# Performance work log

Hardware: AMD Instinct MI355X
Metric: run time of the kernel (lower is better)

The kernel has to match this reference:

```python
import jax, jax.numpy as jnp
import numpy as np
import math

MAX_LEN = 65536
NUM_HEADS = 16
HEAD_DIM = 64
K_MAX = 64
LOCAL_WINDOW = 512
LOG_N = math.ceil(math.log2(MAX_LEN + 1))   # 17
LEAF_START = 2 ** LOG_N                      # segment-tree leaf offset


def cover_set(pos):
    """O(log n) segment-tree nodes covering prefix [0..pos-1], each with leaf-depth."""
    if pos <= 0:
        return []
    l, r = LEAF_START, LEAF_START + min(pos, MAX_LEN)
    out = []
    while l < r:
        if l & 1:
            out.append((l, LOG_N - int(math.floor(math.log2(l)))))
            l += 1
        if r & 1:
            r -= 1
            out.append((r, LOG_N - int(math.floor(math.log2(r)))))
        l >>= 1
        r >>= 1
    return out


def node_content(v_tokens, node_idx, depth):
    """Content of a FULL subtree node under the concat/pairwise-mean gated merge.
    Equals: concat tokens while K<=k_max, then (left+right)/2 elementwise, which
    collapses to a strided mean over chunks of size L//K_MAX. Returns (H, K, D)."""
    L = 1 << depth
    a = (node_idx << depth) - LEAF_START          # first token covered by node
    chunk = v_tokens[a:a + L]                     # (L, H, D), static slice
    if L <= K_MAX:
        f = chunk                                 # (L, H, D)
    else:
        f = chunk.reshape(L // K_MAX, K_MAX, NUM_HEADS, HEAD_DIM).mean(0)  # (K_MAX,H,D)
    return jnp.transpose(f, (1, 0, 2))            # (H, K, D)


def setup_inputs() -> dict:
    key = jax.random.key(0)
    k1, k2, k3 = jax.random.split(key, 3)
    v_tokens = jax.random.normal(k1, (50000, NUM_HEADS, HEAD_DIM), jnp.float32)
    q_new = jax.random.normal(k2, (1, NUM_HEADS, HEAD_DIM), jnp.float32)
    depth_proj_w = jax.random.normal(k3, (LOG_N + 1, HEAD_DIM, HEAD_DIM), jnp.float32) * 0.02
    depth_temp = jnp.linspace(0.5, 4.0, LOG_N + 1).astype(jnp.float32)
    return {"v_tokens": v_tokens, "q_new": q_new, "depth_proj_w": depth_proj_w,
            "depth_temp": depth_temp, "n_tokens": 50000}


def reference(v_tokens, q_new, depth_proj_w, depth_temp, n_tokens):
    pos = int(n_tokens)
    q = q_new[0]                                   # (H, D)
    inv_sqrt_d = 1.0 / math.sqrt(HEAD_DIM)

    # --- local window attention over last min(pos, W) tokens (chronological) ---
    n_local = min(pos, LOCAL_WINDOW)
    v_local = v_tokens[pos - n_local:pos]          # (W, H, D)
    s = jnp.einsum('hd,khd->hk', q, v_local) * inv_sqrt_d
    w = jax.nn.softmax(s, axis=-1)
    local_out = jnp.einsum('hk,khd->hd', w, v_local)   # (H, D)

    # --- multi-depth causal tree attention over the O(log n) cover set ---
    node_outs = []
    for node_idx, depth in cover_set(pos):
        f = node_content(v_tokens, node_idx, depth)    # (H, K, D)
        q_depth = q + q @ depth_proj_w[depth].T        # depth-specific query delta
        scale = 1.0 / ((jax.nn.softplus(depth_temp[depth]) + 1e-6) * math.sqrt(HEAD_DIM))
        s = jnp.einsum('hd,hkd->hk', q_depth, f) * scale
        w = jnp.einsum('hk,hkd->hd', jax.nn.softmax(s, axis=-1), f)
        node_outs.append(w)
    if node_outs:
        tree_out = jnp.stack(node_outs, axis=0).mean(0)
    else:
        tree_out = jnp.zeros_like(local_out)

    return (local_out + tree_out)[None]            # (1, H, D)
```

## Files before the change

### kernel.cpp

```cpp
#include <hip/hip_runtime.h>
#include <math.h>

#define NUM_HEADS   16
#define HEAD_DIM    64
#define KMAXN       64
#define LOCAL_WIN   512
#define LOG_N       17
#define LEAF_START  131072
#define MAX_LEN_TOK 65536
#define ROW         1024
#define SLICE       65536
#define MAXN        34

typedef float vf4 __attribute__((ext_vector_type(4)));

__device__ __forceinline__ vf4 ntload(const float* p) {
    return __builtin_nontemporal_load((const vf4*)p);
}

struct K1Args {
    int nNodes;
    int a[MAXN];
    int cpb[MAXN];
    int C[MAXN];
    int CB[MAXN];
    int K[MAXN];
    int off[MAXN];
    int bbase[MAXN];
};

struct K2Args {
    int nNodes;
    int K[MAXN];
    int C[MAXN];
    int CB[MAXN];
    int off[MAXN];
    int depth[MAXN];
};

__device__ __forceinline__ void f4add(float4& a, const float4& b) {
    a.x += b.x; a.y += b.y; a.z += b.z; a.w += b.w;
}

__global__ __launch_bounds__(256, 4) void k1_reduce(const float* __restrict__ v,
                                                    float* __restrict__ ws,
                                                    K1Args A) {
    int b = blockIdx.x;
    int node = 0;
    for (int i = 1; i < A.nNodes; ++i)
        if (b >= A.bbase[i]) node = i;
    int lb  = b - A.bbase[node];
    int K   = A.K[node];
    int kgc = (K + 3) >> 2;
    int cb  = lb / kgc;
    int kg  = lb - cb * kgc;
    int k0  = kg * 4;
    int RK  = K - k0; if (RK > 4) RK = 4;
    int c0  = cb * A.cpb[node];
    int c1  = c0 + A.cpb[node];
    int C   = A.C[node];
    if (c1 > C) c1 = C;

    int j4 = threadIdx.x * 4;

    vf4 acc0 = 0.f, acc1 = 0.f, acc2 = 0.f, acc3 = 0.f;

    if (RK == 4) {
        int c = c0;
        for (; c + 2 <= c1; c += 2) {
            const float* p0 = v + (long)(A.a[node] + c * 64 + k0) * ROW + j4;
            const float* p1 = p0 + SLICE;
            vf4 y0 = ntload(p0);
            vf4 y1 = ntload(p0 + ROW);
            vf4 y2 = ntload(p0 + 2 * ROW);
            vf4 y3 = ntload(p0 + 3 * ROW);
            vf4 z0 = ntload(p1);
            vf4 z1 = ntload(p1 + ROW);
            vf4 z2 = ntload(p1 + 2 * ROW);
            vf4 z3 = ntload(p1 + 3 * ROW);
            acc0 += y0 + z0; acc1 += y1 + z1; acc2 += y2 + z2; acc3 += y3 + z3;
        }
        if (c < c1) {
            const float* p0 = v + (long)(A.a[node] + c * 64 + k0) * ROW + j4;
            acc0 += ntload(p0);
            acc1 += ntload(p0 + ROW);
            acc2 += ntload(p0 + 2 * ROW);
            acc3 += ntload(p0 + 3 * ROW);
        }
    } else {
        for (int c = c0; c < c1; ++c) {
            const float* p0 = v + (long)(A.a[node] + c * 64 + k0) * ROW + j4;
            if (RK > 0) acc0 += ntload(p0);
            if (RK > 1) acc1 += ntload(p0 + ROW);
            if (RK > 2) acc2 += ntload(p0 + 2 * ROW);
            if (RK > 3) acc3 += ntload(p0 + 3 * ROW);
        }
    }

    float* wp = ws + (long)A.off[node] + (long)cb * SLICE + (long)k0 * ROW + j4;
    if (RK > 0) *(vf4*)(wp)           = acc0;
    if (RK > 1) *(vf4*)(wp + ROW)     = acc1;
    if (RK > 2) *(vf4*)(wp + 2 * ROW) = acc2;
    if (RK > 3) *(vf4*)(wp + 3 * ROW) = acc3;
}

__global__ __launch_bounds__(256) void k1b_finalize(const float* __restrict__ ws_in,
                                                    float* __restrict__ f,
                                                    K2Args A) {
    int node = blockIdx.y;
    int k    = blockIdx.x;
    if (k >= A.K[node]) return;
    int CB = A.CB[node];
    const float* pf = ws_in + (long)A.off[node] + (long)k * ROW + threadIdx.x * 4;
    float4 a0 = make_float4(0.f,0.f,0.f,0.f);
    float4 a1 = a0, a2 = a0, a3 = a0;
    int cb = 0;
    for (; cb + 4 <= CB; cb += 4) {
        f4add(a0, *(const float4*)(pf + (long)cb * SLICE));
        f4add(a1, *(const float4*)(pf + (long)(cb+1) * SLICE));
        f4add(a2, *(const float4*)(pf + (long)(cb+2) * SLICE));
        f4add(a3, *(const float4*)(pf + (long)(cb+3) * SLICE));
    }
    for (; cb < CB; ++cb) f4add(a0, *(const float4*)(pf + (long)cb * SLICE));
    f4add(a0,a1); f4add(a2,a3); f4add(a0,a2);
    float invC = 1.0f / (float)A.C[node];
    a0.x*=invC; a0.y*=invC; a0.z*=invC; a0.w*=invC;
    *(float4*)(f + ((long)node * 64 + k) * ROW + threadIdx.x * 4) = a0;
}

__global__ __launch_bounds__(256) void k2_node_attn(const float* __restrict__ f,
                                                    const float* __restrict__ q,
                                                    const float* __restrict__ W,
                                                    const float* __restrict__ temp,
                                                    float* __restrict__ node_out,
                                                    K2Args A) {
    int h    = blockIdx.x;
    int node = blockIdx.y;
    int lane = threadIdx.x & 63;
    int w    = threadIdx.x >> 6;
    int K    = A.K[node];
    int dep  = A.depth[node];
    const float* pf = f + (long)node * SLICE + h * 64;

    __shared__ float qs[64], qds[64], sv[64], ps[64];
    __shared__ float red[4][64];

    if (threadIdx.x < 64) qs[lane] = q[h * 64 + lane];
    __syncthreads();

    float qp = 0.f;
    const float* Wr = W + ((long)dep * 64 + lane) * 64;
    #pragma unroll
    for (int e = w * 16; e < w * 16 + 16; ++e) qp += qs[e] * Wr[e];
    red[w][lane] = qp;
    __syncthreads();
    if (w == 0) qds[lane] = qs[lane] + red[0][lane] + red[1][lane] + red[2][lane] + red[3][lane];
    __syncthreads();
    float qd = qds[lane];

    float sp    = log1pf(expf(temp[dep]));
    float scale = 1.0f / ((sp + 1e-6f) * 8.0f);

    for (int k = w; k < K; k += 4) {
        float p = qd * pf[(long)k * ROW + lane];
        #pragma unroll
        for (int m = 1; m < 64; m <<= 1) p += __shfl_xor(p, m, 64);
        if (lane == 0) sv[k] = p * scale;
    }
    __syncthreads();

    if (w == 0) {
        float s  = (lane < K) ? sv[lane] : -1e30f;
        float mx = s;
        #pragma unroll
        for (int m = 1; m < 64; m <<= 1) mx = fmaxf(mx, __shfl_xor(mx, m, 64));
        float e = (lane < K) ? expf(s - mx) : 0.f;
        float S = e;
        #pragma unroll
        for (int m = 1; m < 64; m <<= 1) S += __shfl_xor(S, m, 64);
        ps[lane] = e / S;
    }
    __syncthreads();

    float o = 0.f;
    for (int k = w; k < K; k += 4) o += ps[k] * pf[(long)k * ROW + lane];
    red[w][lane] = o;
    __syncthreads();
    if (w == 0)
        node_out[node * ROW + h * 64 + lane] =
            red[0][lane] + red[1][lane] + red[2][lane] + red[3][lane];
}

__global__ __launch_bounds__(512) void k3_local(const float* __restrict__ v,
                                                const float* __restrict__ q,
                                                const float* __restrict__ node_out,
                                                int nNodes, int pos,
                                                float* __restrict__ out) {
    int h    = blockIdx.x;
    int tid  = threadIdx.x;
    int lane = tid & 63;
    int w    = tid >> 6;
    int nloc = pos < LOCAL_WIN ? pos : LOCAL_WIN;
    int t0   = pos - nloc;

    __shared__ float qs[64];
    __shared__ float sc[LOCAL_WIN];
    __shared__ float red[8][64];
    __shared__ float wred[16];
    __shared__ float mS[2];

    if (tid < 64) qs[tid] = q[h * 64 + tid];
    __syncthreads();

    float s = -1e30f;
    if (tid < nloc) {
        const float* vr = v + (long)(t0 + tid) * ROW + h * 64;
        float acc = 0.f;
        #pragma unroll 8
        for (int d = 0; d < 64; ++d) acc += qs[d] * vr[d];
        s = acc * 0.125f;
    }
    float mx = s;
    #pragma unroll
    for (int m = 1; m < 64; m <<= 1) mx = fmaxf(mx, __shfl_xor(mx, m, 64));
    if (lane == 0) wred[w] = mx;
    __syncthreads();
    if (tid == 0) {
        float m2 = wred[0];
        for (int i = 1; i < 8; ++i) m2 = fmaxf(m2, wred[i]);
        mS[0] = m2;
    }
    __syncthreads();
    float m = mS[0];

    float e = (tid < nloc) ? expf(s - m) : 0.f;
    sc[tid] = e;
    float su = e;
    #pragma unroll
    for (int mm = 1; mm < 64; mm <<= 1) su += __shfl_xor(su, mm, 64);
    if (lane == 0) wred[8 + w] = su;
    __syncthreads();
    if (tid == 0) {
        float S2 = 0.f;
        for (int i = 0; i < 8; ++i) S2 += wred[8 + i];
        mS[1] = S2;
    }
    __syncthreads();
    float S = mS[1];

    float acc = 0.f;
    {
        const float* vb = v + (long)t0 * ROW + h * 64 + lane;
        int tb = w * 64;
        #pragma unroll 4
        for (int i = 0; i < 64; ++i) {
            int t = tb + i;
            if (t < nloc) acc += sc[t] * vb[(long)t * ROW];
        }
    }
    red[w][lane] = acc;
    __syncthreads();

    if (w == 0) {
        float tot = 0.f;
        #pragma unroll
        for (int i = 0; i < 8; ++i) tot += red[i][lane];
        tot = (nloc > 0) ? tot / S : 0.f;
        float tr = 0.f;
        for (int n = 0; n < nNodes; ++n) tr += node_out[n * ROW + h * 64 + lane];
        if (nNodes > 0) tr /= (float)nNodes;
        out[h * 64 + lane] = tot + tr;
    }
}

static int floor_log2_host(unsigned x) { int r = 0; while (x >>= 1) ++r; return r; }

extern "C" void kernel_launch(void* const* d_in, const int* in_sizes, int n_in,
                              void* d_out, int out_size, void* d_ws, size_t ws_size,
                              hipStream_t stream) {
    const float* v    = (const float*)d_in[0];
    const float* q    = (const float*)d_in[1];
    const float* W    = (const float*)d_in[2];
    const float* temp = (const float*)d_in[3];
    float* out        = (float*)d_out;
    float* ws         = (float*)d_ws;

    int pos = in_sizes[0] / ROW;

    int n_nodes = 0;
    int nv[MAXN], nd[MAXN];
    if (pos > 0) {
        long l = LEAF_START;
        long r = LEAF_START + (pos < MAX_LEN_TOK ? pos : MAX_LEN_TOK);
        while (l < r) {
            if (l & 1) { nv[n_nodes] = (int)l; nd[n_nodes] = LOG_N - floor_log2_host((unsigned)l); ++n_nodes; ++l; }
            if (r & 1) { --r; nv[n_nodes] = (int)r; nd[n_nodes] = LOG_N - floor_log2_host((unsigned)r); ++n_nodes; }
            l >>= 1; r >>= 1;
        }
    }

    int cpb_choice = 1024;
    for (int cand : {8, 16, 32, 64, 128, 256, 512, 1024}) {
        long tot_cb = 0;
        for (int i = 0; i < n_nodes; ++i) {
            int L = 1 << nd[i];
            int C = (L > KMAXN) ? L / KMAXN : 1;
            tot_cb += (C + cand - 1) / cand;
        }
        long need = ((tot_cb + n_nodes) * (long)SLICE + (long)n_nodes * ROW) * 4;
        if (need <= (long)ws_size) { cpb_choice = cand; break; }
    }

    K1Args A1{}; K2Args A2{};
    A1.nNodes = n_nodes; A2.nNodes = n_nodes;
    int off = 0, bb = 0;
    for (int i = 0; i < n_nodes; ++i) {
        int depth = nd[i];
        int L = 1 << depth;
        int a = (nv[i] << depth) - LEAF_START;
        int K = (L < KMAXN) ? L : KMAXN;
        int C = (L > KMAXN) ? L / KMAXN : 1;
        int CB = (C + cpb_choice - 1) / cpb_choice;
        int cpb = (C + CB - 1) / CB;
        int kgc = (K + 3) / 4;
        A1.a[i] = a;   A1.cpb[i] = cpb; A1.C[i] = C; A1.CB[i] = CB; A1.K[i] = K;
        A1.off[i] = off; A1.bbase[i] = bb;
        A2.K[i] = K;   A2.C[i] = C;    A2.CB[i] = CB;
        A2.off[i] = off; A2.depth[i] = depth;
        off += CB * SLICE;
        bb  += kgc * CB;
    }
    float* f_buf     = ws + (long)off;
    float* node_outp = f_buf + (long)n_nodes * SLICE;

    if (n_nodes > 0) {
        hipLaunchKernelGGL(k1_reduce, dim3(bb), dim3(256), 0, stream, v, ws, A1);
        hipLaunchKernelGGL(k1b_finalize, dim3(64, n_nodes), dim3(256), 0, stream,
                           ws, f_buf, A2);
        hipLaunchKernelGGL(k2_node_attn, dim3(NUM_HEADS, n_nodes), dim3(256), 0, stream,
                           f_buf, q, W, temp, node_outp, A2);
    }
    hipLaunchKernelGGL(k3_local, dim3(NUM_HEADS), dim3(512), 0, stream,
                       v, q, node_outp, n_nodes, pos, out);
}
```

Before: 312.9 us.

## Fuse partial-sum finalize into node attention and parallelize local window

The separate finalize kernel is removed. Each per-head node-attention block now sums the k1 partial slices straight into a shared-memory tile, and small nodes (C==1) read the tokens directly instead of going through the reduce kernel. Local window attention runs as extra blocks in the same grid, so it overlaps with the node blocks, and a tiny combine kernel does the final averaging. This is meant to cut launches and the f buffer's round trip through global memory, but it adds one combine launch and moves the partial-slice reads into more, smaller blocks. The minimum chunks-per-block candidate also rises from 8 to 16.

```diff
diff --git a/kernel.cpp b/kernel.cpp
--- a/kernel.cpp
+++ b/kernel.cpp
@@ -35,12 +35,9 @@
     int C[MAXN];
     int CB[MAXN];
     int off[MAXN];
+    int a[MAXN];
     int depth[MAXN];
 };
-
-__device__ __forceinline__ void f4add(float4& a, const float4& b) {
-    a.x += b.x; a.y += b.y; a.z += b.z; a.w += b.w;
-}
 
 __global__ __launch_bounds__(256, 4) void k1_reduce(const float* __restrict__ v,
                                                     float* __restrict__ ws,
@@ -104,173 +101,185 @@
     if (RK > 3) *(vf4*)(wp + 3 * ROW) = acc3;
 }
 
-__global__ __launch_bounds__(256) void k1b_finalize(const float* __restrict__ ws_in,
-                                                    float* __restrict__ f,
-                                                    K2Args A) {
-    int node = blockIdx.y;
-    int k    = blockIdx.x;
-    if (k >= A.K[node]) return;
-    int CB = A.CB[node];
-    const float* pf = ws_in + (long)A.off[node] + (long)k * ROW + threadIdx.x * 4;
-    float4 a0 = make_float4(0.f,0.f,0.f,0.f);
-    float4 a1 = a0, a2 = a0, a3 = a0;
-    int cb = 0;
-    for (; cb + 4 <= CB; cb += 4) {
-        f4add(a0, *(const float4*)(pf + (long)cb * SLICE));
-        f4add(a1, *(const float4*)(pf + (long)(cb+1) * SLICE));
-        f4add(a2, *(const float4*)(pf + (long)(cb+2) * SLICE));
-        f4add(a3, *(const float4*)(pf + (long)(cb+3) * SLICE));
-    }
-    for (; cb < CB; ++cb) f4add(a0, *(const float4*)(pf + (long)cb * SLICE));
-    f4add(a0,a1); f4add(a2,a3); f4add(a0,a2);
-    float invC = 1.0f / (float)A.C[node];
-    a0.x*=invC; a0.y*=invC; a0.z*=invC; a0.w*=invC;
-    *(float4*)(f + ((long)node * 64 + k) * ROW + threadIdx.x * 4) = a0;
-}
-
-__global__ __launch_bounds__(256) void k2_node_attn(const float* __restrict__ f,
-                                                    const float* __restrict__ q,
-                                                    const float* __restrict__ W,
-                                                    const float* __restrict__ temp,
-                                                    float* __restrict__ node_out,
-                                                    K2Args A) {
+__global__ __launch_bounds__(512) void k2_fused(const float* __restrict__ v,
+                                                const float* __restrict__ ws,
+                                                const float* __restrict__ q,
+                                                const float* __restrict__ W,
+                                                const float* __restrict__ temp,
+                                                float* __restrict__ node_out,
+                                                float* __restrict__ local_out,
+                                                int pos, K2Args A) {
     int h    = blockIdx.x;
     int node = blockIdx.y;
-    int lane = threadIdx.x & 63;
-    int w    = threadIdx.x >> 6;
-    int K    = A.K[node];
-    int dep  = A.depth[node];
-    const float* pf = f + (long)node * SLICE + h * 64;
-
+    int tid  = threadIdx.x;
+    int lane = tid & 63;
+    int w    = tid >> 6;
+
+    __shared__ float fh[64][64];
     __shared__ float qs[64], qds[64], sv[64], ps[64];
-    __shared__ float red[4][64];
-
-    if (threadIdx.x < 64) qs[lane] = q[h * 64 + lane];
-    __syncthreads();
-
-    float qp = 0.f;
-    const float* Wr = W + ((long)dep * 64 + lane) * 64;
-    #pragma unroll
-    for (int e = w * 16; e < w * 16 + 16; ++e) qp += qs[e] * Wr[e];
-    red[w][lane] = qp;
-    __syncthreads();
-    if (w == 0) qds[lane] = qs[lane] + red[0][lane] + red[1][lane] + red[2][lane] + red[3][lane];
-    __syncthreads();
-    float qd = qds[lane];
-
-    float sp    = log1pf(expf(temp[dep]));
-    float scale = 1.0f / ((sp + 1e-6f) * 8.0f);
-
-    for (int k = w; k < K; k += 4) {
-        float p = qd * pf[(long)k * ROW + lane];
+    __shared__ float red[8][64];
+    __shared__ float sc[LOCAL_WIN];
+    __shared__ float wred[16];
+    __shared__ float mS[2];
+
+    if (node < A.nNodes) {
+        int K = A.K[node];
+        if (tid < 64) qs[tid] = q[h * 64 + tid];
+
+        const float* bp; int CB; float invC;
+        if (A.C[node] > 1) {
+            bp   = ws + (long)A.off[node] + h * 64;
+            CB   = A.CB[node];
+            invC = 1.0f / (float)A.C[node];
+        } else {
+            bp   = v + (long)A.a[node] * ROW + h * 64;
+            CB   = 1;
+            invC = 1.0f;
+        }
+        for (int id = tid; id < 1024; id += 512) {
+            int r  = id >> 4;
+            int c4 = (id & 15) << 2;
+            if (r < K) {
+                vf4 s0 = 0.f, s1 = 0.f, s2 = 0.f, s3 = 0.f;
+                const float* p = bp + (long)r * ROW + c4;
+                int cb = 0;
+                for (; cb + 4 <= CB; cb += 4) {
+                    s0 += *(const vf4*)(p + (long)cb * SLICE);
+                    s1 += *(const vf4*)(p + (long)(cb + 1) * SLICE);
+                    s2 += *(const vf4*)(p + (long)(cb + 2) * SLICE);
+                    s3 += *(const vf4*)(p + (long)(cb + 3) * SLICE);
+                }
+                for (; cb < CB; ++cb) s0 += *(const vf4*)(p + (long)cb * SLICE);
+                s0 += s1; s2 += s3; s0 += s2;
+                s0 *= invC;
+                *(vf4*)&fh[r][c4] = s0;
+            }
+        }
+        __syncthreads();
+
+        int dep = A.depth[node];
+        float qp = 0.f;
+        const float* Wr = W + ((long)dep * 64 + lane) * 64;
         #pragma unroll
-        for (int m = 1; m < 64; m <<= 1) p += __shfl_xor(p, m, 64);
-        if (lane == 0) sv[k] = p * scale;
-    }
-    __syncthreads();
-
-    if (w == 0) {
-        float s  = (lane < K) ? sv[lane] : -1e30f;
+        for (int e = w * 8; e < w * 8 + 8; ++e) qp += qs[e] * Wr[e];
+        red[w][lane] = qp;
+        __syncthreads();
+        if (w == 0) {
+            float t = qs[lane];
+            #pragma unroll
+            for (int i = 0; i < 8; ++i) t += red[i][lane];
+            qds[lane] = t;
+        }
+        __syncthreads();
+        float qd    = qds[lane];
+        float sp    = log1pf(expf(temp[dep]));
+        float scale = 1.0f / ((sp + 1e-6f) * 8.0f);
+
+        for (int k = w; k < K; k += 8) {
+            float p = qd * fh[k][lane];
+            #pragma unroll
+            for (int m = 1; m < 64; m <<= 1) p += __shfl_xor(p, m, 64);
+            if (lane == 0) sv[k] = p * scale;
+        }
+        __syncthreads();
+
+        if (w == 0) {
+            float s  = (lane < K) ? sv[lane] : -1e30f;
+            float mx = s;
+            #pragma unroll
+            for (int m = 1; m < 64; m <<= 1) mx = fmaxf(mx, __shfl_xor(mx, m, 64));
+            float e = (lane < K) ? expf(s - mx) : 0.f;
+            float S = e;
+            #pragma unroll
+            for (int m = 1; m < 64; m <<= 1) S += __shfl_xor(S, m, 64);
+            ps[lane] = e / S;
+        }
+        __syncthreads();
+
+        float o = 0.f;
+        for (int k = w; k < K; k += 8) o += ps[k] * fh[k][lane];
+        red[w][lane] = o;
+        __syncthreads();
+        if (w == 0) {
+            float t = 0.f;
+            #pragma unroll
+            for (int i = 0; i < 8; ++i) t += red[i][lane];
+            node_out[node * ROW + h * 64 + lane] = t;
+        }
+    } else {
+        int nloc = pos < LOCAL_WIN ? pos : LOCAL_WIN;
+        int t0   = pos - nloc;
+
+        if (tid < 64) qs[tid] = q[h * 64 + tid];
+        __syncthreads();
+
+        float s = -1e30f;
+        if (tid < nloc) {
+            const float* vr = v + (long)(t0 + tid) * ROW + h * 64;
+            float acc = 0.f;
+            #pragma unroll 8
+            for (int d = 0; d < 64; ++d) acc += qs[d] * vr[d];
+            s = acc * 0.125f;
+        }
         float mx = s;
         #pragma unroll
         for (int m = 1; m < 64; m <<= 1) mx = fmaxf(mx, __shfl_xor(mx, m, 64));
-        float e = (lane < K) ? expf(s - mx) : 0.f;
-        float S = e;
+        if (lane == 0) wred[w] = mx;
+        __syncthreads();
+        if (tid == 0) {
+            float m2 = wred[0];
+            for (int i = 1; i < 8; ++i) m2 = fmaxf(m2, wred[i]);
+            mS[0] = m2;
+        }
+        __syncthreads();
+        float m = mS[0];
+
+        float e = (tid < nloc) ? expf(s - m) : 0.f;
+        sc[tid] = e;
+        float su = e;
         #pragma unroll
-        for (int m = 1; m < 64; m <<= 1) S += __shfl_xor(S, m, 64);
-        ps[lane] = e / S;
-    }
-    __syncthreads();
-
-    float o = 0.f;
-    for (int k = w; k < K; k += 4) o += ps[k] * pf[(long)k * ROW + lane];
-    red[w][lane] = o;
-    __syncthreads();
-    if (w == 0)
-        node_out[node * ROW + h * 64 + lane] =
-            red[0][lane] + red[1][lane] + red[2][lane] + red[3][lane];
-}
-
-__global__ __launch_bounds__(512) void k3_local(const float* __restrict__ v,
-                                                const float* __restrict__ q,
-                                                const float* __restrict__ node_out,
-                                                int nNodes, int pos,
-                                                float* __restrict__ out) {
-    int h    = blockIdx.x;
-    int tid  = threadIdx.x;
-    int lane = tid & 63;
-    int w    = tid >> 6;
-    int nloc = pos < LOCAL_WIN ? pos : LOCAL_WIN;
-    int t0   = pos - nloc;
-
-    __shared__ float qs[64];
-    __shared__ float sc[LOCAL_WIN];
-    __shared__ float red[8][64];
-    __shared__ float wred[16];
-    __shared__ float mS[2];
-
-    if (tid < 64) qs[tid] = q[h * 64 + tid];
-    __syncthreads();
-
-    float s = -1e30f;
-    if (tid < nloc) {
-        const float* vr = v + (long)(t0 + tid) * ROW + h * 64;
+        for (int mm = 1; mm < 64; mm <<= 1) su += __shfl_xor(su, mm, 64);
+        if (lane == 0) wred[8 + w] = su;
+        __syncthreads();
+        if (tid == 0) {
+            float S2 = 0.f;
+            for (int i = 0; i < 8; ++i) S2 += wred[8 + i];
+            mS[1] = S2;
+        }
+        __syncthreads();
+        float S = mS[1];
+
         float acc = 0.f;
-        #pragma unroll 8
-        for (int d = 0; d < 64; ++d) acc += qs[d] * vr[d];
-        s = acc * 0.125f;
-    }
-    float mx = s;
-    #pragma unroll
-    for (int m = 1; m < 64; m <<= 1) mx = fmaxf(mx, __shfl_xor(mx, m, 64));
-    if (lane == 0) wred[w] = mx;
-    __syncthreads();
-    if (tid == 0) {
-        float m2 = wred[0];
-        for (int i = 1; i < 8; ++i) m2 = fmaxf(m2, wred[i]);
-        mS[0] = m2;
-    }
-    __syncthreads();
-    float m = mS[0];
-
-    float e = (tid < nloc) ? expf(s - m) : 0.f;
-    sc[tid] = e;
-    float su = e;
-    #pragma unroll
-    for (int mm = 1; mm < 64; mm <<= 1) su += __shfl_xor(su, mm, 64);
-    if (lane == 0) wred[8 + w] = su;
-    __syncthreads();
-    if (tid == 0) {
-        float S2 = 0.f;
-        for (int i = 0; i < 8; ++i) S2 += wred[8 + i];
-        mS[1] = S2;
-    }
-    __syncthreads();
-    float S = mS[1];
-
-    float acc = 0.f;
-    {
-        const float* vb = v + (long)t0 * ROW + h * 64 + lane;
-        int tb = w * 64;
-        #pragma unroll 4
-        for (int i = 0; i < 64; ++i) {
-            int t = tb + i;
-            if (t < nloc) acc += sc[t] * vb[(long)t * ROW];
-        }
-    }
-    red[w][lane] = acc;
-    __syncthreads();
-
-    if (w == 0) {
-        float tot = 0.f;
-        #pragma unroll
-        for (int i = 0; i < 8; ++i) tot += red[i][lane];
-        tot = (nloc > 0) ? tot / S : 0.f;
-        float tr = 0.f;
-        for (int n = 0; n < nNodes; ++n) tr += node_out[n * ROW + h * 64 + lane];
-        if (nNodes > 0) tr /= (float)nNodes;
-        out[h * 64 + lane] = tot + tr;
-    }
+        {
+            const float* vb = v + (long)t0 * ROW + h * 64 + lane;
+            int tb = w * 64;
+            #pragma unroll 4
+            for (int i = 0; i < 64; ++i) {
+                int t = tb + i;
+                if (t < nloc) acc += sc[t] * vb[(long)t * ROW];
+            }
+        }
+        red[w][lane] = acc;
+        __syncthreads();
+
+        if (w == 0) {
+            float tot = 0.f;
+            #pragma unroll
+            for (int i = 0; i < 8; ++i) tot += red[i][lane];
+            local_out[h * 64 + lane] = (nloc > 0) ? tot / S : 0.f;
+        }
+    }
+}
+
+__global__ __launch_bounds__(256) void k3_combine(const float* __restrict__ node_out,
+                                                  const float* __restrict__ local_out,
+                                                  int nNodes,
+                                                  float* __restrict__ out) {
+    int i = blockIdx.x * 256 + threadIdx.x;
+    float tr = 0.f;
+    for (int n = 0; n < nNodes; ++n) tr += node_out[(long)n * ROW + i];
+    if (nNodes > 0) tr /= (float)nNodes;
+    out[i] = local_out[i] + tr;
 }
 
 static int floor_log2_host(unsigned x) { int r = 0; while (x >>= 1) ++r; return r; }
@@ -300,46 +309,51 @@
     }
 
     int cpb_choice = 1024;
-    for (int cand : {8, 16, 32, 64, 128, 256, 512, 1024}) {
+    for (int cand : {16, 32, 64, 128, 256, 512, 1024}) {
         long tot_cb = 0;
         for (int i = 0; i < n_nodes; ++i) {
             int L = 1 << nd[i];
             int C = (L > KMAXN) ? L / KMAXN : 1;
-            tot_cb += (C + cand - 1) / cand;
-        }
-        long need = ((tot_cb + n_nodes) * (long)SLICE + (long)n_nodes * ROW) * 4;
+            if (C > 1) tot_cb += (C + cand - 1) / cand;
+        }
+        long need = (tot_cb * (long)SLICE + (long)n_nodes * ROW + ROW) * 4;
         if (need <= (long)ws_size) { cpb_choice = cand; break; }
     }
 
     K1Args A1{}; K2Args A2{};
-    A1.nNodes = n_nodes; A2.nNodes = n_nodes;
-    int off = 0, bb = 0;
+    A2.nNodes = n_nodes;
+    int off = 0, bb = 0, nBig = 0;
     for (int i = 0; i < n_nodes; ++i) {
         int depth = nd[i];
         int L = 1 << depth;
         int a = (nv[i] << depth) - LEAF_START;
         int K = (L < KMAXN) ? L : KMAXN;
         int C = (L > KMAXN) ? L / KMAXN : 1;
-        int CB = (C + cpb_choice - 1) / cpb_choice;
-        int cpb = (C + CB - 1) / CB;
-        int kgc = (K + 3) / 4;
-        A1.a[i] = a;   A1.cpb[i] = cpb; A1.C[i] = C; A1.CB[i] = CB; A1.K[i] = K;
-        A1.off[i] = off; A1.bbase[i] = bb;
-        A2.K[i] = K;   A2.C[i] = C;    A2.CB[i] = CB;
-        A2.off[i] = off; A2.depth[i] = depth;
-        off += CB * SLICE;
-        bb  += kgc * CB;
-    }
-    float* f_buf     = ws + (long)off;
-    float* node_outp = f_buf + (long)n_nodes * SLICE;
-
-    if (n_nodes > 0) {
+        A2.K[i] = K; A2.C[i] = C; A2.a[i] = a; A2.depth[i] = depth;
+        if (C > 1) {
+            int CB  = (C + cpb_choice - 1) / cpb_choice;
+            int cpb = (C + CB - 1) / CB;
+            int kgc = (K + 3) / 4;
+            A1.a[nBig] = a;   A1.cpb[nBig] = cpb; A1.C[nBig] = C;
+            A1.CB[nBig] = CB; A1.K[nBig] = K;
+            A1.off[nBig] = off; A1.bbase[nBig] = bb;
+            A2.CB[i] = CB; A2.off[i] = off;
+            off += CB * SLICE;
+            bb  += kgc * CB;
+            ++nBig;
+        } else {
+            A2.CB[i] = 1; A2.off[i] = 0;
+        }
+    }
+    A1.nNodes = nBig;
+
+    float* node_outp  = ws + (long)off;
+    float* local_outp = node_outp + (long)n_nodes * ROW;
+
+    if (nBig > 0)
         hipLaunchKernelGGL(k1_reduce, dim3(bb), dim3(256), 0, stream, v, ws, A1);
-        hipLaunchKernelGGL(k1b_finalize, dim3(64, n_nodes), dim3(256), 0, stream,
-                           ws, f_buf, A2);
-        hipLaunchKernelGGL(k2_node_attn, dim3(NUM_HEADS, n_nodes), dim3(256), 0, stream,
-                           f_buf, q, W, temp, node_outp, A2);
-    }
-    hipLaunchKernelGGL(k3_local, dim3(NUM_HEADS), dim3(512), 0, stream,
-                       v, q, node_outp, n_nodes, pos, out);
-}
+    hipLaunchKernelGGL(k2_fused, dim3(NUM_HEADS, n_nodes + 1), dim3(512), 0, stream,
+                       v, ws, q, W, temp, node_outp, local_outp, pos, A2);
+    hipLaunchKernelGGL(k3_combine, dim3(4), dim3(256), 0, stream,
+                       node_outp, local_outp, n_nodes, out);
+}
```

Result: faster. 291.8 us (-6.7%).
